# Kernel optimization log

Hardware: AMD Instinct MI355X
Metric: run time of the kernel (lower is better)

## Reference

```python
import jax, jax.numpy as jnp
import numpy as np
import math

D = 2048          # embedding_size
H = 16            # nheads
HD = D // H       # head_dim
S = 2048          # seq_len
B = 2
# SwiGLU hidden per source: int(2*(4*D)/3) rounded up to multiple of 256
FF = 256 * ((int(2 * (4 * D) / 3) + 255) // 256)  # 5632
EPS = 1e-6


def pe_row(seq_len, d_model):
    # PositionalEncoding buffer, but forward uses only pe[:, seq_len-1]
    pos = float(seq_len - 1)
    div = jnp.exp(jnp.arange(0, d_model, 2, dtype=jnp.float32) * (-math.log(10000.0) / d_model))
    row = jnp.zeros((d_model,), jnp.float32)
    row = row.at[0::2].set(jnp.sin(pos * div))
    row = row.at[1::2].set(jnp.cos(pos * div))
    return row  # [D]


def rmsnorm(x, g, eps=EPS):
    xf = x.astype(jnp.float32)
    n = xf * jax.lax.rsqrt(jnp.mean(xf * xf, axis=-1, keepdims=True) + eps)
    return g * n.astype(x.dtype)


def setup_inputs() -> dict:
    key = jax.random.key(0)
    ks = jax.random.split(key, 16)
    sd = 0.02
    x = jax.random.normal(ks[0], (B, S, D), jnp.float32)
    mask = jnp.triu(jnp.ones((S, S), jnp.int32), k=1)[None, None]  # [1,1,S,S], 1 = masked
    return {
        'x': x,
        'mask': mask,
        'qkv_w': jax.random.normal(ks[1], (3 * D, D), jnp.float32) * sd,
        'qkv_b': jnp.zeros((3 * D,), jnp.float32),
        'fc_w': jax.random.normal(ks[2], (D, D), jnp.float32) * sd,
        'fc_b': jnp.zeros((D,), jnp.float32),
        'w1': jax.random.normal(ks[3], (FF, D), jnp.float32) * sd,
        'b1': jnp.zeros((FF,), jnp.float32),
        'w2': jax.random.normal(ks[4], (FF, D), jnp.float32) * sd,
        'b2': jnp.zeros((FF,), jnp.float32),
        'w3': jax.random.normal(ks[5], (D, FF), jnp.float32) * sd,
        'b3': jnp.zeros((D,), jnp.float32),
        'g_attn': jnp.ones((D,), jnp.float32),
        'g_ff': jnp.ones((D,), jnp.float32),
    }


def _block(x, mask, qkv_w, qkv_b, fc_w, fc_b, w1, b1, w2, b2, w3, b3, g_attn, g_ff):
    b, s, _ = x.shape
    # attention sublayer (pre-norm)
    h_in = rmsnorm(x, g_attn)
    qkv = h_in @ qkv_w.T + qkv_b
    xq, xk, xv = jnp.split(qkv, 3, axis=-1)
    pe = pe_row(s, D)  # single row added everywhere (faithful to source)
    xq = xq + pe
    xk = xk + pe
    q = xq.reshape(b, s, H, HD).transpose(0, 2, 1, 3)
    k = xk.reshape(b, s, H, HD).transpose(0, 2, 1, 3)
    v = xv.reshape(b, s, H, HD).transpose(0, 2, 1, 3)
    scores = jnp.einsum('bhqd,bhkd->bhqk', q, k) / math.sqrt(HD)
    scores = jnp.where(mask == 1, jnp.float32(-1e9), scores)
    attn = jax.nn.softmax(scores, axis=-1)
    out = jnp.einsum('bhqk,bhkd->bhqd', attn, v)
    out = out.transpose(0, 2, 1, 3).reshape(b, s, D)
    attn_out = out @ fc_w.T + fc_b
    h = x + attn_out
    # SwiGLU FFN sublayer (pre-norm)
    f_in = rmsnorm(h, g_ff)
    gate = jax.nn.silu(f_in @ w1.T + b1) * (f_in @ w2.T + b2)
    return h + gate @ w3.T + b3


def reference(x, mask, qkv_w, qkv_b, fc_w, fc_b, w1, b1, w2, b2, w3, b3, g_attn, g_ff):
    return _block(x, mask, qkv_w, qkv_b, fc_w, fc_b, w1, b1, w2, b2, w3, b3, g_attn, g_ff)
```

## Files before the change

kernel.cpp:

```cpp
#include <hip/hip_runtime.h>
#include <math.h>


typedef __attribute__((ext_vector_type(8))) short bf16x8;
typedef __attribute__((ext_vector_type(4))) short bf16x4;
typedef __attribute__((ext_vector_type(4))) float f32x4;

#define DEVI __device__ __forceinline__

DEVI unsigned short f2bf(float f) {
  unsigned u = __builtin_bit_cast(unsigned, f);
  u += 0x7FFFu + ((u >> 16) & 1u);
  return (unsigned short)(u >> 16);
}
DEVI float bf2f(unsigned short h) {
  unsigned u = ((unsigned)h) << 16;
  return __builtin_bit_cast(float, u);
}

#define GLL16(g, l) __builtin_amdgcn_global_load_lds( \
    (const __attribute__((address_space(1))) unsigned int*)(const void*)(g), \
    (__attribute__((address_space(3))) unsigned int*)(void*)(l), 16, 0, 0)

__global__ __launch_bounds__(256) void wconv5_k(const float* __restrict__ s0, unsigned short* __restrict__ d0,
                                                const float* __restrict__ s1, unsigned short* __restrict__ d1,
                                                const float* __restrict__ s2, unsigned short* __restrict__ d2,
                                                const float* __restrict__ s3, unsigned short* __restrict__ d3,
                                                const float* __restrict__ s4, unsigned short* __restrict__ d4) {
  long bid = blockIdx.x;
  const float* src; unsigned short* dst; long base;
  if (bid < 6144)       { src = s0; dst = d0; base = bid; }
  else if (bid < 8192)  { src = s1; dst = d1; base = bid - 6144; }
  else if (bid < 13824) { src = s2; dst = d2; base = bid - 8192; }
  else if (bid < 19456) { src = s3; dst = d3; base = bid - 13824; }
  else                  { src = s4; dst = d4; base = bid - 19456; }
  long t = base * 256 + threadIdx.x;
  const f32x4* s = (const f32x4*)(src + t * 8);
  f32x4 a = s[0], b = s[1];
  bf16x8 o;
#pragma unroll
  for (int j = 0; j < 4; ++j) {
    o[j]     = (short)f2bf(a[j]);
    o[4 + j] = (short)f2bf(b[j]);
  }
  *(bf16x8*)(dst + t * 8) = o;
}

__global__ void pe_k(float* __restrict__ pe) {
  int c = blockIdx.x * 256 + threadIdx.x;
  if (c >= 2048) return;
  int i2 = c & ~1;
  float div = __expf(-(float)i2 * (9.210340371976184f / 2048.0f));
  float ang = 2047.0f * div;
  pe[c] = (c & 1) ? cosf(ang) : sinf(ang);
}

__global__ __launch_bounds__(256) void rmsnorm_k(const float* __restrict__ x,
                                                 const float* __restrict__ g,
                                                 unsigned short* __restrict__ out) {
  long row = blockIdx.x;
  const float* xr = x + row * 2048;
  int tid = threadIdx.x;
  f32x4 v0 = *(const f32x4*)&xr[tid * 8];
  f32x4 v1 = *(const f32x4*)&xr[tid * 8 + 4];
  float ss = 0.f;
#pragma unroll
  for (int j = 0; j < 4; ++j) ss += v0[j] * v0[j] + v1[j] * v1[j];
#pragma unroll
  for (int m = 1; m < 64; m <<= 1) ss += __shfl_xor(ss, m, 64);
  __shared__ float red[4];
  int lane = tid & 63, wv = tid >> 6;
  if (lane == 0) red[wv] = ss;
  __syncthreads();
  float tot = red[0] + red[1] + red[2] + red[3];
  float rn = rsqrtf(tot * (1.0f / 2048.0f) + 1e-6f);
  const float* gr = g + tid * 8;
  bf16x8 o;
#pragma unroll
  for (int j = 0; j < 4; ++j) {
    o[j]     = (short)f2bf(v0[j] * rn * gr[j]);
    o[4 + j] = (short)f2bf(v1[j] * rn * gr[4 + j]);
  }
  *(bf16x8*)&out[row * 2048 + tid * 8] = o;
}

template <int EPI>
__global__ __launch_bounds__(256) void gemm_bt(const unsigned short* __restrict__ A,
                                               const unsigned short* __restrict__ W,
                                               const float* __restrict__ bias,
                                               const void* __restrict__ residv,
                                               void* __restrict__ outv,
                                               int M, int N, int K) {
  __shared__ __align__(16) unsigned short Ab[3][4096];
  __shared__ __align__(16) unsigned short Bb[3][4096];
  const int tid  = threadIdx.x;
  const int lane = tid & 63;
  const int wv   = tid >> 6;
  const int wr   = wv >> 1;
  const int wc   = wv & 1;
  const int l15  = lane & 15;
  const int lg   = lane >> 4;
  const long tm  = (long)blockIdx.y * 128;
  const long tn  = (long)blockIdx.x * 128;

  const int srw = tid >> 2;
  const int sch = ((tid & 3) ^ ((srw >> 1) & 3)) << 3;
  const unsigned short* gA = A + (tm + srw) * (long)K + sch;
  const unsigned short* gB = W + (tn + srw) * (long)K + sch;
  const long rowstep = 64L * K;

#define STG(slot, kt) do {                                          \
    GLL16(gA + ((long)(kt) << 5), &Ab[slot][wv * 512]);             \
    GLL16(gA + rowstep + ((long)(kt) << 5), &Ab[slot][2048 + wv * 512]); \
    GLL16(gB + ((long)(kt) << 5), &Bb[slot][wv * 512]);             \
    GLL16(gB + rowstep + ((long)(kt) << 5), &Bb[slot][2048 + wv * 512]); \
  } while (0)

  const int KT = K >> 5;
  STG(0, 0); STG(1, 1);
  asm volatile("s_waitcnt vmcnt(4)" ::: "memory");
  __builtin_amdgcn_s_barrier();

  f32x4 acc[4][4] = {};
  const int sw = ((lg ^ ((l15 >> 1) & 3)) << 3);

  for (int t = 0; t < KT; ++t) {
    const unsigned short* lA = &Ab[t % 3][0];
    const unsigned short* lB = &Bb[t % 3][0];
    bf16x8 af[4], bfv[4];
#pragma unroll
    for (int m = 0; m < 4; ++m)
      af[m] = *(const bf16x8*)&lA[(wr * 64 + m * 16 + l15) * 32 + sw];
#pragma unroll
    for (int n = 0; n < 4; ++n)
      bfv[n] = *(const bf16x8*)&lB[(wc * 64 + n * 16 + l15) * 32 + sw];
    if (t + 2 < KT) STG((t + 2) % 3, t + 2);
    __builtin_amdgcn_s_setprio(1);
#pragma unroll
    for (int m = 0; m < 4; ++m)
#pragma unroll
      for (int n = 0; n < 4; ++n)
        acc[m][n] = __builtin_amdgcn_mfma_f32_16x16x32_bf16(af[m], bfv[n], acc[m][n], 0, 0, 0);
    __builtin_amdgcn_s_setprio(0);
    if (t + 2 < KT)      asm volatile("s_waitcnt vmcnt(4)" ::: "memory");
    else if (t + 1 < KT) asm volatile("s_waitcnt vmcnt(0)" ::: "memory");
    __builtin_amdgcn_s_barrier();
  }
#undef STG
  __builtin_amdgcn_sched_barrier(0);

  const long row0 = tm + wr * 64 + ((lane >> 4) << 2);
  const long col0 = tn + wc * 64;
#pragma unroll
  for (int n = 0; n < 4; ++n) {
    const long col = col0 + n * 16 + l15;
    const float bv = bias[col];
#pragma unroll
    for (int m = 0; m < 4; ++m) {
      const long rw = row0 + m * 16;
#pragma unroll
      for (int j = 0; j < 4; ++j) {
        const float v = acc[m][n][j] + bv;
        const long i = (rw + j) * (long)N + col;
        if (EPI == 0) {
          ((unsigned short*)outv)[i] = f2bf(v);
        } else if (EPI == 1) {
          ((float*)outv)[i] = ((const float*)residv)[i] + v;
        } else {
          float f1 = bf2f(((const unsigned short*)residv)[i]);
          float sg = f1 / (1.0f + __expf(-f1));
          ((unsigned short*)outv)[i] = f2bf(sg * v);
        }
      }
    }
  }
}

__global__ __launch_bounds__(256) void krepack_k(const unsigned short* __restrict__ qkv,
                                                 const float* __restrict__ pe,
                                                 unsigned short* __restrict__ kpe) {
  long t = (long)blockIdx.x * 256 + threadIdx.x;
  long idx = t * 8;
  long row = idx >> 11;
  int cd  = (int)(idx & 2047);
  int h = cd >> 7, d = cd & 127;
  long b = row >> 11, s = row & 2047;
  bf16x8 v = *(const bf16x8*)&qkv[row * 6144 + 2048 + cd];
  const float* per = &pe[cd];
#pragma unroll
  for (int j = 0; j < 8; ++j)
    v[j] = (short)f2bf(bf2f((unsigned short)v[j]) + per[j]);
  *(bf16x8*)&kpe[(((b * 16 + h)) * 2048 + s) * 128 + d] = v;
}

__global__ __launch_bounds__(256) void vtrans_k(const unsigned short* __restrict__ qkv,
                                                unsigned short* __restrict__ Vt) {
  const int s0 = blockIdx.x * 64;
  const int d0 = blockIdx.y * 64;
  const int bh = blockIdx.z;
  const long b = bh >> 4;
  const int h = bh & 15;
  __shared__ unsigned short tile[64][76];
  const int t = threadIdx.x;
#pragma unroll
  for (int half = 0; half < 2; ++half) {
    int c = t + half * 256;
    int r = c >> 3;
    int cc = (c & 7) * 8;
    bf16x8 v = *(const bf16x8*)&qkv[(b * 2048 + s0 + r) * 6144 + 4096 + h * 128 + d0 + cc];
#pragma unroll
    for (int j = 0; j < 8; ++j) tile[cc + j][r] = (unsigned short)v[j];
  }
  __syncthreads();
#pragma unroll
  for (int half = 0; half < 2; ++half) {
    int c = t + half * 256;
    int dr = c >> 3;
    int sc = (c & 7) * 8;
    bf16x4 lo = *(const bf16x4*)&tile[dr][sc];
    bf16x4 hi = *(const bf16x4*)&tile[dr][sc + 4];
    bf16x8 v;
#pragma unroll
    for (int j = 0; j < 4; ++j) { v[j] = lo[j]; v[4 + j] = hi[j]; }
    *(bf16x8*)&Vt[((long)bh * 128 + d0 + dr) * 2048 + s0 + sc] = v;
  }
}

__global__ __launch_bounds__(256, 2) void fattn_k(const unsigned short* __restrict__ QKV,
                                                  const float* __restrict__ pe,
                                                  const unsigned short* __restrict__ Kp,
                                                  const unsigned short* __restrict__ Vt,
                                                  unsigned short* __restrict__ O) {
  const int lin = blockIdx.x;
  const int chunk = lin & 7;
  const int idx = lin >> 3;
  const int bh = chunk * 4 + (idx >> 4);
  const int i16 = idx & 15;
  const int qb = (i16 & 1) ? ((i16 - 1) >> 1) : (15 - (i16 >> 1));
  const long b = bh >> 4;
  const int h = bh & 15;
  const int q0 = qb * 128;
  const int tid = threadIdx.x, lane = tid & 63, wv = tid >> 6;
  const int l15 = lane & 15, lg = lane >> 4;
  const int qw = q0 + wv * 32;

  __shared__ __align__(16) unsigned short Kl[2][8192];
  __shared__ __align__(16) unsigned short Vl[2][8192];
  __shared__ __align__(16) unsigned short Plds[4][32][44];

  const float scale = 0.08838834764831845f;
  const unsigned short* Qb = QKV + (b * 2048 + qw) * 6144 + h * 128;
  bf16x8 qf[2][4];
#pragma unroll
  for (int r = 0; r < 2; ++r)
#pragma unroll
    for (int kc = 0; kc < 4; ++kc) {
      bf16x8 v = *(const bf16x8*)&Qb[(r * 16 + l15) * 6144 + kc * 32 + lg * 8];
      const float* per = &pe[h * 128 + kc * 32 + lg * 8];
#pragma unroll
      for (int j = 0; j < 8; ++j)
        v[j] = (short)f2bf((bf2f((unsigned short)v[j]) + per[j]) * scale);
      qf[r][kc] = v;
    }

  const unsigned short* Kg = Kp + (long)bh * 2048 * 128;
  const unsigned short* Vg = Vt + (long)bh * 128 * 2048;

  auto stage = [&](int buf, int key0) {
#pragma unroll
    for (int ld = 0; ld < 4; ++ld) {
      int sr = wv * 16 + ld * 4 + (lane >> 4);
      int sc = ((lane & 15) << 3) ^ ((sr & 7) << 3);
      GLL16(Kg + (long)(key0 + sr) * 128 + sc, &Kl[buf][wv * 2048 + ld * 512]);
      int dr = wv * 32 + ld * 8 + (lane >> 3);
      int dc = ((lane & 7) << 3) ^ ((dr & 7) << 3);
      GLL16(Vg + (long)dr * 2048 + key0 + dc, &Vl[buf][wv * 2048 + ld * 512]);
    }
  };

  f32x4 o[2][8] = {};
  float mr[2][4], sdn[2][4];
#pragma unroll
  for (int r = 0; r < 2; ++r)
#pragma unroll
    for (int j = 0; j < 4; ++j) { mr[r][j] = -1e30f; sdn[r][j] = 0.f; }

  const int nkt = (q0 >> 6) + 2;
  stage(0, 0);
  __syncthreads();
  int cur = 0;
  for (int kt = 0; kt < nkt; ++kt) {
    const int key0 = kt << 6;
    if (kt + 1 < nkt) stage(cur ^ 1, key0 + 64);
    if (key0 <= qw + 31) {
      f32x4 s[2][4] = {};
      __builtin_amdgcn_s_setprio(1);
#pragma unroll
      for (int ks = 0; ks < 4; ++ks) {
        bf16x8 kf[4];
#pragma unroll
        for (int kc = 0; kc < 4; ++kc)
          kf[kc] = *(const bf16x8*)&Kl[cur][(ks * 16 + l15) * 128 +
                                           ((kc * 32 + lg * 8) ^ ((l15 & 7) << 3))];
#pragma unroll
        for (int r = 0; r < 2; ++r)
#pragma unroll
          for (int kc = 0; kc < 4; ++kc)
            s[r][ks] = __builtin_amdgcn_mfma_f32_16x16x32_bf16(qf[r][kc], kf[kc], s[r][ks], 0, 0, 0);
      }
      __builtin_amdgcn_s_setprio(0);
      const bool maskt = (key0 + 63 > qw);
      float pm[2][4];
#pragma unroll
      for (int r = 0; r < 2; ++r)
#pragma unroll
        for (int j = 0; j < 4; ++j) pm[r][j] = -1e30f;
#pragma unroll
      for (int r = 0; r < 2; ++r)
#pragma unroll
        for (int ks = 0; ks < 4; ++ks)
#pragma unroll
          for (int j = 0; j < 4; ++j) {
            float v = s[r][ks][j];
            if (maskt) {
              int qrow = qw + r * 16 + lg * 4 + j;
              int key  = key0 + ks * 16 + l15;
              v = (key <= qrow) ? v : -1e30f;
              s[r][ks][j] = v;
            }
            pm[r][j] = fmaxf(pm[r][j], v);
          }
#pragma unroll
      for (int msk = 1; msk < 16; msk <<= 1)
#pragma unroll
        for (int r = 0; r < 2; ++r)
#pragma unroll
          for (int j = 0; j < 4; ++j) pm[r][j] = fmaxf(pm[r][j], __shfl_xor(pm[r][j], msk, 64));
      bool grow = false;
#pragma unroll
      for (int r = 0; r < 2; ++r)
#pragma unroll
        for (int j = 0; j < 4; ++j) grow = grow || (pm[r][j] > mr[r][j] + 8.0f);
      if (__any(grow)) {
#pragma unroll
        for (int r = 0; r < 2; ++r)
#pragma unroll
          for (int j = 0; j < 4; ++j) {
            float mn = fmaxf(mr[r][j], pm[r][j]);
            float corr = __expf(mr[r][j] - mn);
            mr[r][j] = mn;
            sdn[r][j] *= corr;
#pragma unroll
            for (int nf = 0; nf < 8; ++nf) o[r][nf][j] *= corr;
          }
      }
      float ps[2][4];
#pragma unroll
      for (int r = 0; r < 2; ++r)
#pragma unroll
        for (int j = 0; j < 4; ++j) ps[r][j] = 0.f;
#pragma unroll
      for (int r = 0; r < 2; ++r)
#pragma unroll
        for (int ks = 0; ks < 4; ++ks)
#pragma unroll
          for (int j = 0; j < 4; ++j) {
            float e = __expf(s[r][ks][j] - mr[r][j]);
            s[r][ks][j] = e;
            ps[r][j] += e;
          }
#pragma unroll
      for (int msk = 1; msk < 16; msk <<= 1)
#pragma unroll
        for (int r = 0; r < 2; ++r)
#pragma unroll
          for (int j = 0; j < 4; ++j) ps[r][j] += __shfl_xor(ps[r][j], msk, 64);
#pragma unroll
      for (int r = 0; r < 2; ++r)
#pragma unroll
        for (int j = 0; j < 4; ++j) sdn[r][j] += ps[r][j];
#pragma unroll
      for (int hk = 0; hk < 2; ++hk) {
#pragma unroll
        for (int r = 0; r < 2; ++r)
#pragma unroll
          for (int ks2 = 0; ks2 < 2; ++ks2)
#pragma unroll
            for (int j = 0; j < 4; ++j)
              Plds[wv][r * 16 + lg * 4 + j][ks2 * 16 + l15] = f2bf(s[r][hk * 2 + ks2][j]);
        bf16x8 pf[2];
#pragma unroll
        for (int r = 0; r < 2; ++r) {
          bf16x4 lo = *(const bf16x4*)&Plds[wv][r * 16 + l15][lg * 8];
          bf16x4 hi = *(const bf16x4*)&Plds[wv][r * 16 + l15][lg * 8 + 4];
          bf16x8 p;
#pragma unroll
          for (int j = 0; j < 4; ++j) { p[j] = lo[j]; p[4 + j] = hi[j]; }
          pf[r] = p;
        }
        __builtin_amdgcn_s_setprio(1);
#pragma unroll
        for (int nf = 0; nf < 8; ++nf) {
          bf16x8 vf = *(const bf16x8*)&Vl[cur][(nf * 16 + l15) * 64 +
                                              ((hk * 32 + lg * 8) ^ ((l15 & 7) << 3))];
#pragma unroll
          for (int r = 0; r < 2; ++r)
            o[r][nf] = __builtin_amdgcn_mfma_f32_16x16x32_bf16(pf[r], vf, o[r][nf], 0, 0, 0);
        }
        __builtin_amdgcn_s_setprio(0);
      }
    }
    __syncthreads();
    cur ^= 1;
  }
  unsigned short* Ob = O + (b * 2048 + qw) * 2048 + h * 128;
#pragma unroll
  for (int r = 0; r < 2; ++r)
#pragma unroll
    for (int j = 0; j < 4; ++j) {
      float inv = 1.0f / sdn[r][j];
#pragma unroll
      for (int nf = 0; nf < 8; ++nf)
        Ob[(long)(r * 16 + lg * 4 + j) * 2048 + nf * 16 + l15] = f2bf(o[r][nf][j] * inv);
    }
}

extern "C" void kernel_launch(void* const* d_in, const int* in_sizes, int n_in,
                              void* d_out, int out_size, void* d_ws, size_t ws_size,
                              hipStream_t stream) {
  (void)in_sizes; (void)n_in; (void)out_size; (void)ws_size;
  const float* x    = (const float*)d_in[0];
  const float* qkvw = (const float*)d_in[2];
  const float* qkvb = (const float*)d_in[3];
  const float* fcw  = (const float*)d_in[4];
  const float* fcb  = (const float*)d_in[5];
  const float* w1   = (const float*)d_in[6];
  const float* b1   = (const float*)d_in[7];
  const float* w2   = (const float*)d_in[8];
  const float* b2   = (const float*)d_in[9];
  const float* w3   = (const float*)d_in[10];
  const float* b3   = (const float*)d_in[11];
  const float* ga   = (const float*)d_in[12];
  const float* gf   = (const float*)d_in[13];

  char* ws = (char*)d_ws;
  size_t off = 0;
  auto alloc = [&](size_t bytes) -> char* {
    char* p = ws + off;
    off = (off + bytes + 255) & ~(size_t)255;
    return p;
  };
  unsigned short* wqkv  = (unsigned short*)alloc(6144L * 2048 * 2);
  unsigned short* wfc   = (unsigned short*)alloc(2048L * 2048 * 2);
  unsigned short* w1b   = (unsigned short*)alloc(5632L * 2048 * 2);
  unsigned short* w2b   = (unsigned short*)alloc(5632L * 2048 * 2);
  unsigned short* w3b   = (unsigned short*)alloc(2048L * 5632 * 2);
  float*          pe    = (float*)alloc(2048 * 4);
  unsigned short* hin   = (unsigned short*)alloc(4096L * 2048 * 2);
  unsigned short* qkv   = (unsigned short*)alloc(4096L * 6144 * 2);
  unsigned short* kpe   = (unsigned short*)alloc(4096L * 2048 * 2);
  unsigned short* Vt    = (unsigned short*)alloc(4096L * 2048 * 2);
  unsigned short* attnb = (unsigned short*)alloc(4096L * 2048 * 2);
  float* h = (float*)d_out;

  wconv5_k<<<25088, 256, 0, stream>>>(qkvw, wqkv, fcw, wfc, w1, w1b, w2, w2b, w3, w3b);
  pe_k<<<8, 256, 0, stream>>>(pe);

  rmsnorm_k<<<4096, 256, 0, stream>>>(x, ga, hin);
  gemm_bt<0><<<dim3(48, 32), 256, 0, stream>>>(hin, wqkv, qkvb, nullptr, qkv, 4096, 6144, 2048);
  krepack_k<<<4096, 256, 0, stream>>>(qkv, pe, kpe);
  vtrans_k<<<dim3(32, 2, 32), 256, 0, stream>>>(qkv, Vt);
  fattn_k<<<dim3(512), 256, 0, stream>>>(qkv, pe, kpe, Vt, attnb);
  gemm_bt<1><<<dim3(16, 32), 256, 0, stream>>>(attnb, wfc, fcb, x, h, 4096, 2048, 2048);

  rmsnorm_k<<<4096, 256, 0, stream>>>(h, gf, hin);
  unsigned short* a1 = qkv;
  gemm_bt<0><<<dim3(44, 32), 256, 0, stream>>>(hin, w1b, b1, nullptr, a1, 4096, 5632, 2048);
  gemm_bt<2><<<dim3(44, 32), 256, 0, stream>>>(hin, w2b, b2, a1, a1, 4096, 5632, 2048);
  gemm_bt<1><<<dim3(16, 32), 256, 0, stream>>>(a1, w3b, b3, h, d_out, 4096, 2048, 5632);
}
```

Measured before the change: 750.5 us.

## Restructure flash attention to 8-wave blocks processing paired causal query tiles

The attention kernel now launches 256 blocks of 512 threads, each wave handling 16 query rows instead of 32. Each block processes two query tiles in sequence, a long one (15-p) and a short one (p), so every block does equal causal work and there are no tail imbalances. With 256 blocks there is one per CU and each K/V stage is shared by eight waves, but each wave does half the MFMA work per K/V fragment load. The serial two-segment loop with one block per CU may lose latency hiding compared with two blocks per CU.

```diff
diff --git a/kernel.cpp b/kernel.cpp
--- a/kernel.cpp
+++ b/kernel.cpp
@@ -226,203 +226,166 @@
   }
 }
 
-__global__ __launch_bounds__(256, 2) void fattn_k(const unsigned short* __restrict__ QKV,
+__global__ __launch_bounds__(512, 1) void fattn_k(const unsigned short* __restrict__ QKV,
                                                   const float* __restrict__ pe,
                                                   const unsigned short* __restrict__ Kp,
                                                   const unsigned short* __restrict__ Vt,
                                                   unsigned short* __restrict__ O) {
   const int lin = blockIdx.x;
   const int chunk = lin & 7;
-  const int idx = lin >> 3;
-  const int bh = chunk * 4 + (idx >> 4);
-  const int i16 = idx & 15;
-  const int qb = (i16 & 1) ? ((i16 - 1) >> 1) : (15 - (i16 >> 1));
+  const int j4 = lin >> 3;
+  const int bh = chunk * 4 + (j4 >> 3);
+  const int p  = j4 & 7;
   const long b = bh >> 4;
   const int h = bh & 15;
-  const int q0 = qb * 128;
   const int tid = threadIdx.x, lane = tid & 63, wv = tid >> 6;
   const int l15 = lane & 15, lg = lane >> 4;
-  const int qw = q0 + wv * 32;
 
   __shared__ __align__(16) unsigned short Kl[2][8192];
   __shared__ __align__(16) unsigned short Vl[2][8192];
-  __shared__ __align__(16) unsigned short Plds[4][32][44];
+  __shared__ __align__(16) unsigned short Plds[8][16][44];
 
   const float scale = 0.08838834764831845f;
-  const unsigned short* Qb = QKV + (b * 2048 + qw) * 6144 + h * 128;
-  bf16x8 qf[2][4];
-#pragma unroll
-  for (int r = 0; r < 2; ++r)
+  const unsigned short* Kg = Kp + (long)bh * 2048 * 128;
+  const unsigned short* Vg = Vt + (long)bh * 128 * 2048;
+
+  auto stage = [&](int buf, int key0) {
+#pragma unroll
+    for (int ld = 0; ld < 2; ++ld) {
+      int sr = wv * 8 + ld * 4 + (lane >> 4);
+      int sc = ((lane & 15) << 3) ^ ((sr & 7) << 3);
+      GLL16(Kg + (long)(key0 + sr) * 128 + sc, &Kl[buf][wv * 1024 + ld * 512]);
+      int dr = wv * 16 + ld * 8 + (lane >> 3);
+      int dc = ((lane & 7) << 3) ^ ((dr & 7) << 3);
+      GLL16(Vg + (long)dr * 2048 + key0 + dc, &Vl[buf][wv * 1024 + ld * 512]);
+    }
+  };
+
+  for (int seg = 0; seg < 2; ++seg) {
+    const int qb = (seg == 0) ? (15 - p) : p;
+    const int q0 = qb * 128;
+    const int qw = q0 + wv * 16;
+
+    const unsigned short* Qb = QKV + (b * 2048 + qw) * 6144 + h * 128;
+    bf16x8 qf[4];
 #pragma unroll
     for (int kc = 0; kc < 4; ++kc) {
-      bf16x8 v = *(const bf16x8*)&Qb[(r * 16 + l15) * 6144 + kc * 32 + lg * 8];
+      bf16x8 v = *(const bf16x8*)&Qb[l15 * 6144 + kc * 32 + lg * 8];
       const float* per = &pe[h * 128 + kc * 32 + lg * 8];
 #pragma unroll
       for (int j = 0; j < 8; ++j)
         v[j] = (short)f2bf((bf2f((unsigned short)v[j]) + per[j]) * scale);
-      qf[r][kc] = v;
+      qf[kc] = v;
     }
 
-  const unsigned short* Kg = Kp + (long)bh * 2048 * 128;
-  const unsigned short* Vg = Vt + (long)bh * 128 * 2048;
-
-  auto stage = [&](int buf, int key0) {
-#pragma unroll
-    for (int ld = 0; ld < 4; ++ld) {
-      int sr = wv * 16 + ld * 4 + (lane >> 4);
-      int sc = ((lane & 15) << 3) ^ ((sr & 7) << 3);
-      GLL16(Kg + (long)(key0 + sr) * 128 + sc, &Kl[buf][wv * 2048 + ld * 512]);
-      int dr = wv * 32 + ld * 8 + (lane >> 3);
-      int dc = ((lane & 7) << 3) ^ ((dr & 7) << 3);
-      GLL16(Vg + (long)dr * 2048 + key0 + dc, &Vl[buf][wv * 2048 + ld * 512]);
-    }
-  };
-
-  f32x4 o[2][8] = {};
-  float mr[2][4], sdn[2][4];
-#pragma unroll
-  for (int r = 0; r < 2; ++r)
-#pragma unroll
-    for (int j = 0; j < 4; ++j) { mr[r][j] = -1e30f; sdn[r][j] = 0.f; }
-
-  const int nkt = (q0 >> 6) + 2;
-  stage(0, 0);
-  __syncthreads();
-  int cur = 0;
-  for (int kt = 0; kt < nkt; ++kt) {
-    const int key0 = kt << 6;
-    if (kt + 1 < nkt) stage(cur ^ 1, key0 + 64);
-    if (key0 <= qw + 31) {
-      f32x4 s[2][4] = {};
-      __builtin_amdgcn_s_setprio(1);
-#pragma unroll
-      for (int ks = 0; ks < 4; ++ks) {
-        bf16x8 kf[4];
-#pragma unroll
-        for (int kc = 0; kc < 4; ++kc)
-          kf[kc] = *(const bf16x8*)&Kl[cur][(ks * 16 + l15) * 128 +
-                                           ((kc * 32 + lg * 8) ^ ((l15 & 7) << 3))];
-#pragma unroll
-        for (int r = 0; r < 2; ++r)
+    f32x4 o[8] = {};
+    float mr[4] = {-1e30f, -1e30f, -1e30f, -1e30f};
+    float sdn[4] = {0.f, 0.f, 0.f, 0.f};
+
+    const int nkt = (q0 >> 6) + 2;
+    stage(0, 0);
+    __syncthreads();
+    int cur = 0;
+    for (int kt = 0; kt < nkt; ++kt) {
+      const int key0 = kt << 6;
+      if (kt + 1 < nkt) stage(cur ^ 1, key0 + 64);
+      if (key0 <= qw + 15) {
+        f32x4 s[4] = {};
+        __builtin_amdgcn_s_setprio(1);
+#pragma unroll
+        for (int ks = 0; ks < 4; ++ks) {
+          bf16x8 kf[4];
 #pragma unroll
           for (int kc = 0; kc < 4; ++kc)
-            s[r][ks] = __builtin_amdgcn_mfma_f32_16x16x32_bf16(qf[r][kc], kf[kc], s[r][ks], 0, 0, 0);
-      }
-      __builtin_amdgcn_s_setprio(0);
-      const bool maskt = (key0 + 63 > qw);
-      float pm[2][4];
-#pragma unroll
-      for (int r = 0; r < 2; ++r)
-#pragma unroll
-        for (int j = 0; j < 4; ++j) pm[r][j] = -1e30f;
-#pragma unroll
-      for (int r = 0; r < 2; ++r)
+            kf[kc] = *(const bf16x8*)&Kl[cur][(ks * 16 + l15) * 128 +
+                                             ((kc * 32 + lg * 8) ^ ((l15 & 7) << 3))];
+#pragma unroll
+          for (int kc = 0; kc < 4; ++kc)
+            s[ks] = __builtin_amdgcn_mfma_f32_16x16x32_bf16(qf[kc], kf[kc], s[ks], 0, 0, 0);
+        }
+        __builtin_amdgcn_s_setprio(0);
+        const bool maskt = (key0 + 63 > qw);
+        float pm[4] = {-1e30f, -1e30f, -1e30f, -1e30f};
 #pragma unroll
         for (int ks = 0; ks < 4; ++ks)
 #pragma unroll
           for (int j = 0; j < 4; ++j) {
-            float v = s[r][ks][j];
+            float v = s[ks][j];
             if (maskt) {
-              int qrow = qw + r * 16 + lg * 4 + j;
+              int qrow = qw + lg * 4 + j;
               int key  = key0 + ks * 16 + l15;
               v = (key <= qrow) ? v : -1e30f;
-              s[r][ks][j] = v;
+              s[ks][j] = v;
             }
-            pm[r][j] = fmaxf(pm[r][j], v);
+            pm[j] = fmaxf(pm[j], v);
           }
 #pragma unroll
-      for (int msk = 1; msk < 16; msk <<= 1)
-#pragma unroll
-        for (int r = 0; r < 2; ++r)
-#pragma unroll
-          for (int j = 0; j < 4; ++j) pm[r][j] = fmaxf(pm[r][j], __shfl_xor(pm[r][j], msk, 64));
-      bool grow = false;
-#pragma unroll
-      for (int r = 0; r < 2; ++r)
-#pragma unroll
-        for (int j = 0; j < 4; ++j) grow = grow || (pm[r][j] > mr[r][j] + 8.0f);
-      if (__any(grow)) {
-#pragma unroll
-        for (int r = 0; r < 2; ++r)
+        for (int msk = 1; msk < 16; msk <<= 1)
+#pragma unroll
+          for (int j = 0; j < 4; ++j) pm[j] = fmaxf(pm[j], __shfl_xor(pm[j], msk, 64));
+        bool grow = false;
+#pragma unroll
+        for (int j = 0; j < 4; ++j) grow = grow || (pm[j] > mr[j] + 8.0f);
+        if (__any(grow)) {
 #pragma unroll
           for (int j = 0; j < 4; ++j) {
-            float mn = fmaxf(mr[r][j], pm[r][j]);
-            float corr = __expf(mr[r][j] - mn);
-            mr[r][j] = mn;
-            sdn[r][j] *= corr;
-#pragma unroll
-            for (int nf = 0; nf < 8; ++nf) o[r][nf][j] *= corr;
+            float mn = fmaxf(mr[j], pm[j]);
+            float corr = __expf(mr[j] - mn);
+            mr[j] = mn;
+            sdn[j] *= corr;
+#pragma unroll
+            for (int nf = 0; nf < 8; ++nf) o[nf][j] *= corr;
           }
+        }
+        float ps[4] = {0.f, 0.f, 0.f, 0.f};
+#pragma unroll
+        for (int ks = 0; ks < 4; ++ks)
+#pragma unroll
+          for (int j = 0; j < 4; ++j) {
+            float e = __expf(s[ks][j] - mr[j]);
+            s[ks][j] = e;
+            ps[j] += e;
+          }
+#pragma unroll
+        for (int msk = 1; msk < 16; msk <<= 1)
+#pragma unroll
+          for (int j = 0; j < 4; ++j) ps[j] += __shfl_xor(ps[j], msk, 64);
+#pragma unroll
+        for (int j = 0; j < 4; ++j) sdn[j] += ps[j];
+#pragma unroll
+        for (int hk = 0; hk < 2; ++hk) {
+#pragma unroll
+          for (int ks2 = 0; ks2 < 2; ++ks2)
+#pragma unroll
+            for (int j = 0; j < 4; ++j)
+              Plds[wv][lg * 4 + j][ks2 * 16 + l15] = f2bf(s[hk * 2 + ks2][j]);
+          bf16x4 lo = *(const bf16x4*)&Plds[wv][l15][lg * 8];
+          bf16x4 hi = *(const bf16x4*)&Plds[wv][l15][lg * 8 + 4];
+          bf16x8 pf;
+#pragma unroll
+          for (int j = 0; j < 4; ++j) { pf[j] = lo[j]; pf[4 + j] = hi[j]; }
+          __builtin_amdgcn_s_setprio(1);
+#pragma unroll
+          for (int nf = 0; nf < 8; ++nf) {
+            bf16x8 vf = *(const bf16x8*)&Vl[cur][(nf * 16 + l15) * 64 +
+                                                ((hk * 32 + lg * 8) ^ ((l15 & 7) << 3))];
+            o[nf] = __builtin_amdgcn_mfma_f32_16x16x32_bf16(pf, vf, o[nf], 0, 0, 0);
+          }
+          __builtin_amdgcn_s_setprio(0);
+        }
       }
-      float ps[2][4];
-#pragma unroll
-      for (int r = 0; r < 2; ++r)
-#pragma unroll
-        for (int j = 0; j < 4; ++j) ps[r][j] = 0.f;
-#pragma unroll
-      for (int r = 0; r < 2; ++r)
-#pragma unroll
-        for (int ks = 0; ks < 4; ++ks)
-#pragma unroll
-          for (int j = 0; j < 4; ++j) {
-            float e = __expf(s[r][ks][j] - mr[r][j]);
-            s[r][ks][j] = e;
-            ps[r][j] += e;
-          }
-#pragma unroll
-      for (int msk = 1; msk < 16; msk <<= 1)
-#pragma unroll
-        for (int r = 0; r < 2; ++r)
-#pragma unroll
-          for (int j = 0; j < 4; ++j) ps[r][j] += __shfl_xor(ps[r][j], msk, 64);
-#pragma unroll
-      for (int r = 0; r < 2; ++r)
-#pragma unroll
-        for (int j = 0; j < 4; ++j) sdn[r][j] += ps[r][j];
-#pragma unroll
-      for (int hk = 0; hk < 2; ++hk) {
-#pragma unroll
-        for (int r = 0; r < 2; ++r)
-#pragma unroll
-          for (int ks2 = 0; ks2 < 2; ++ks2)
-#pragma unroll
-            for (int j = 0; j < 4; ++j)
-              Plds[wv][r * 16 + lg * 4 + j][ks2 * 16 + l15] = f2bf(s[r][hk * 2 + ks2][j]);
-        bf16x8 pf[2];
-#pragma unroll
-        for (int r = 0; r < 2; ++r) {
-          bf16x4 lo = *(const bf16x4*)&Plds[wv][r * 16 + l15][lg * 8];
-          bf16x4 hi = *(const bf16x4*)&Plds[wv][r * 16 + l15][lg * 8 + 4];
-          bf16x8 p;
-#pragma unroll
-          for (int j = 0; j < 4; ++j) { p[j] = lo[j]; p[4 + j] = hi[j]; }
-          pf[r] = p;
-        }
-        __builtin_amdgcn_s_setprio(1);
-#pragma unroll
-        for (int nf = 0; nf < 8; ++nf) {
-          bf16x8 vf = *(const bf16x8*)&Vl[cur][(nf * 16 + l15) * 64 +
-                                              ((hk * 32 + lg * 8) ^ ((l15 & 7) << 3))];
-#pragma unroll
-          for (int r = 0; r < 2; ++r)
-            o[r][nf] = __builtin_amdgcn_mfma_f32_16x16x32_bf16(pf[r], vf, o[r][nf], 0, 0, 0);
-        }
-        __builtin_amdgcn_s_setprio(0);
-      }
+      __syncthreads();
+      cur ^= 1;
     }
-    __syncthreads();
-    cur ^= 1;
-  }
-  unsigned short* Ob = O + (b * 2048 + qw) * 2048 + h * 128;
-#pragma unroll
-  for (int r = 0; r < 2; ++r)
+    unsigned short* Ob = O + (b * 2048 + qw) * 2048 + h * 128;
 #pragma unroll
     for (int j = 0; j < 4; ++j) {
-      float inv = 1.0f / sdn[r][j];
+      float inv = 1.0f / sdn[j];
 #pragma unroll
       for (int nf = 0; nf < 8; ++nf)
-        Ob[(long)(r * 16 + lg * 4 + j) * 2048 + nf * 16 + l15] = f2bf(o[r][nf][j] * inv);
+        Ob[(long)(lg * 4 + j) * 2048 + nf * 16 + l15] = f2bf(o[nf][j] * inv);
     }
+  }
 }
 
 extern "C" void kernel_launch(void* const* d_in, const int* in_sizes, int n_in,
@@ -470,7 +433,7 @@
   gemm_bt<0><<<dim3(48, 32), 256, 0, stream>>>(hin, wqkv, qkvb, nullptr, qkv, 4096, 6144, 2048);
   krepack_k<<<4096, 256, 0, stream>>>(qkv, pe, kpe);
   vtrans_k<<<dim3(32, 2, 32), 256, 0, stream>>>(qkv, Vt);
-  fattn_k<<<dim3(512), 256, 0, stream>>>(qkv, pe, kpe, Vt, attnb);
+  fattn_k<<<dim3(256), 512, 0, stream>>>(qkv, pe, kpe, Vt, attnb);
   gemm_bt<1><<<dim3(16, 32), 256, 0, stream>>>(attnb, wfc, fcb, x, h, 4096, 2048, 2048);
 
   rmsnorm_k<<<4096, 256, 0, stream>>>(h, gf, hin);
```

Result: faster. 719.1 us (-4.2%).
